# Performance work log

Measured on AMD Instinct MI355X. Metric: run time of the kernel, lower is better.

## Reference

```python
import jax, jax.numpy as jnp
import numpy as np
import math

NUM_LAYERS = 2
NUM_HEADS = 8
D_MODEL = 256
D_FF = 4 * D_MODEL
FACTOR = 5
B, L, F_IN = 8, 2048, 32


def layer_norm(x, g, b, eps=1e-5):
    m = x.mean(-1, keepdims=True)
    v = ((x - m) ** 2).mean(-1, keepdims=True)
    return (x - m) * jax.lax.rsqrt(v + eps) * g + b


def prob_attention(q, k, v, idx):
    # q,k,v: [B,H,L,Dh]; idx: [L,S] sampled key indices per query (ProbSparse)
    Bq, H, Lq, Dh = q.shape
    u = min(FACTOR * math.ceil(math.log(Lq)), Lq)  # number of 'active' queries
    k_s = k[:, :, idx, :]                              # [B,H,L,S,Dh] gathered keys
    qk_s = jnp.einsum('bhld,bhlsd->bhls', q, k_s)      # sampled scores
    M = qk_s.max(-1) - qk_s.sum(-1) / Lq               # sparsity measure [B,H,L]
    _, top = jax.lax.top_k(M, u)                       # [B,H,u] active query idx
    q_red = jnp.take_along_axis(q, top[..., None], axis=2)   # [B,H,u,Dh]
    scores = jnp.einsum('bhud,bhld->bhul', q_red, k) * (1.0 / math.sqrt(Dh))
    attn = jax.nn.softmax(scores, axis=-1)             # [B,H,u,L]
    upd = jnp.einsum('bhul,bhld->bhud', attn, v)       # [B,H,u,Dh]
    # initial context = mean of V (mask_flag=False), then scatter active rows
    ctx = jnp.broadcast_to(v.mean(2, keepdims=True), (Bq, H, Lq, Dh))
    bi = jnp.arange(Bq)[:, None, None]
    hi = jnp.arange(H)[None, :, None]
    return ctx.at[bi, hi, top].set(upd)


def setup_inputs() -> dict:
    key = jax.random.key(0)
    ks = jax.random.split(key, 16)
    S = min(FACTOR * math.ceil(math.log(L)), L)  # 40
    std = 0.02

    def w(k, shape):
        return jax.random.normal(k, shape, jnp.float32) * std

    inp = {}
    inp['x'] = jax.random.normal(ks[0], (B, L, F_IN), jnp.float32)
    inp['idx_sample'] = jax.random.randint(ks[1], (NUM_LAYERS, L, S), 0, L)
    inp['w_in'] = w(ks[2], (F_IN, D_MODEL)); inp['b_in'] = jnp.zeros((D_MODEL,), jnp.float32)
    inp['wq'] = w(ks[3], (NUM_LAYERS, D_MODEL, D_MODEL)); inp['bq'] = jnp.zeros((NUM_LAYERS, D_MODEL), jnp.float32)
    inp['wk'] = w(ks[4], (NUM_LAYERS, D_MODEL, D_MODEL)); inp['bk'] = jnp.zeros((NUM_LAYERS, D_MODEL), jnp.float32)
    inp['wv'] = w(ks[5], (NUM_LAYERS, D_MODEL, D_MODEL)); inp['bv'] = jnp.zeros((NUM_LAYERS, D_MODEL), jnp.float32)
    inp['wo'] = w(ks[6], (NUM_LAYERS, D_MODEL, D_MODEL)); inp['bo'] = jnp.zeros((NUM_LAYERS, D_MODEL), jnp.float32)
    inp['w_ff1'] = w(ks[7], (NUM_LAYERS, D_MODEL, D_FF)); inp['b_ff1'] = jnp.zeros((NUM_LAYERS, D_FF), jnp.float32)
    inp['w_ff2'] = w(ks[8], (NUM_LAYERS, D_FF, D_MODEL)); inp['b_ff2'] = jnp.zeros((NUM_LAYERS, D_MODEL), jnp.float32)
    inp['ln1_g'] = jnp.ones((NUM_LAYERS, D_MODEL), jnp.float32); inp['ln1_b'] = jnp.zeros((NUM_LAYERS, D_MODEL), jnp.float32)
    inp['ln2_g'] = jnp.ones((NUM_LAYERS, D_MODEL), jnp.float32); inp['ln2_b'] = jnp.zeros((NUM_LAYERS, D_MODEL), jnp.float32)
    inp['w_fc1'] = w(ks[9], (D_MODEL, 64)); inp['b_fc1'] = jnp.zeros((64,), jnp.float32)
    inp['w_fc2'] = w(ks[10], (64, 1)); inp['b_fc2'] = jnp.zeros((1,), jnp.float32)
    return inp


def reference(x, idx_sample, w_in, b_in, wq, bq, wk, bk, wv, bv, wo, bo,
              w_ff1, b_ff1, w_ff2, b_ff2, ln1_g, ln1_b, ln2_g, ln2_b,
              w_fc1, b_fc1, w_fc2, b_fc2):
    Bx, Lx, _ = x.shape
    h = x @ w_in + b_in  # [B,L,D_MODEL]
    for i in range(NUM_LAYERS):
        q = (h @ wq[i] + bq[i]).reshape(Bx, Lx, NUM_HEADS, -1).transpose(0, 2, 1, 3)
        k = (h @ wk[i] + bk[i]).reshape(Bx, Lx, NUM_HEADS, -1).transpose(0, 2, 1, 3)
        v = (h @ wv[i] + bv[i]).reshape(Bx, Lx, NUM_HEADS, -1).transpose(0, 2, 1, 3)
        ctx = prob_attention(q, k, v, idx_sample[i])            # [B,H,L,Dh]
        ctx = ctx.transpose(0, 2, 1, 3).reshape(Bx, Lx, D_MODEL)
        new_x = ctx @ wo[i] + bo[i]
        h = layer_norm(h + new_x, ln1_g[i], ln1_b[i])
        y = jax.nn.relu(h @ w_ff1[i] + b_ff1[i]) @ w_ff2[i] + b_ff2[i]
        h = layer_norm(h + y, ln2_g[i], ln2_b[i])
    last = h[:, -1, :]                      # take final time step
    out = jax.nn.relu(last @ w_fc1 + b_fc1) @ w_fc2 + b_fc2
    return out[:, None, :]                  # unsqueeze(1) -> [B,1,output_size]
```

## Files before the change

### kernel.cpp

```cpp
#include <hip/hip_runtime.h>
#include <math.h>

#define BB 8
#define LL 2048
#define DM 256
#define NH 8
#define DH 32
#define DFF 1024
#define SS 40
#define UU 40
#define BL (BB*LL)
#define NSL 8

typedef unsigned short ushort_t;
typedef __attribute__((ext_vector_type(8))) short short8;
typedef __attribute__((ext_vector_type(4))) float f32x4;

__device__ inline ushort_t f2b(float f)
{
    unsigned int u = __float_as_uint(f);
    u += 0x7fff + ((u >> 16) & 1);
    return (ushort_t)(u >> 16);
}

__device__ inline void gload16(const void* g, const void* l)
{
    __builtin_amdgcn_global_load_lds(
        (const __attribute__((address_space(1))) unsigned int*)g,
        (__attribute__((address_space(3))) unsigned int*)l, 16, 0, 0);
}

template<int RELU, int OUT_MODE>
__global__ __launch_bounds__(256)
void gemm_mfma(const ushort_t* __restrict__ A, const ushort_t* __restrict__ Bt,
               const float* __restrict__ bias, void* __restrict__ Cout,
               void* __restrict__ aux, int M, int N, int K)
{
    __shared__ ushort_t Asl[128 * 32];
    __shared__ ushort_t Bsl[128 * 32];

    const int t    = threadIdx.x;
    const int lane = t & 63;
    const int wv   = t >> 6;
    const int row0 = blockIdx.x * 128;
    const int col0 = blockIdx.y * 128;
    const int wr   = (wv >> 1) * 64;
    const int wc   = (wv & 1) * 64;
    const int quad = lane >> 4;
    const int l16  = lane & 15;

    f32x4 acc[4][4];
    #pragma unroll
    for (int i = 0; i < 4; ++i)
        #pragma unroll
        for (int j = 0; j < 4; ++j)
            acc[i][j] = 0.f;

    for (int k0 = 0; k0 < K; k0 += 32) {
        __syncthreads();
        #pragma unroll
        for (int r = 0; r < 2; ++r) {
            int g = r * 256 + t;
            const ushort_t* ga = A  + (size_t)(row0 + (g >> 2)) * K + k0 + (g & 3) * 8;
            const ushort_t* gb = Bt + (size_t)(col0 + (g >> 2)) * K + k0 + (g & 3) * 8;
            int lbase = (r * 256 + wv * 64) * 16;
            gload16(ga, (const char*)Asl + lbase);
            gload16(gb, (const char*)Bsl + lbase);
        }
        __syncthreads();

        short8 af[4], bfr[4];
        #pragma unroll
        for (int mi = 0; mi < 4; ++mi)
            af[mi] = *(const short8*)&Asl[(wr + mi * 16 + l16) * 32 + quad * 8];
        #pragma unroll
        for (int ni = 0; ni < 4; ++ni)
            bfr[ni] = *(const short8*)&Bsl[(wc + ni * 16 + l16) * 32 + quad * 8];
        #pragma unroll
        for (int mi = 0; mi < 4; ++mi)
            #pragma unroll
            for (int ni = 0; ni < 4; ++ni)
                acc[mi][ni] = __builtin_amdgcn_mfma_f32_16x16x32_bf16(
                    af[mi], bfr[ni], acc[mi][ni], 0, 0, 0);
    }

    #pragma unroll
    for (int mi = 0; mi < 4; ++mi) {
        #pragma unroll
        for (int ni = 0; ni < 4; ++ni) {
            int col = col0 + wc + ni * 16 + l16;
            float bb = bias[col];
            #pragma unroll
            for (int r = 0; r < 4; ++r) {
                int row = row0 + wr + mi * 16 + quad * 4 + r;
                float v = acc[mi][ni][r] + bb;
                if (RELU) v = v > 0.f ? v : 0.f;
                if (OUT_MODE == 0) {
                    ((float*)Cout)[(size_t)row * N + col] = v;
                } else if (OUT_MODE == 1) {
                    int tensor = col >> 8;
                    int c2 = col & 255;
                    int b  = row >> 11, l = row & (LL - 1);
                    int hh = c2 >> 5,  dh = c2 & 31;
                    int bh = b * NH + hh;
                    size_t bi = (((size_t)bh * LL + l) << 5) + dh;
                    ((float*)Cout)[(size_t)tensor * (BB*NH*LL*DH) + bi] = v;
                    if (tensor == 1)
                        ((ushort_t*)aux)[(((size_t)l << 6) + bh) * 32 + dh] = f2b(v);
                } else if (OUT_MODE == 2) {
                    ((ushort_t*)Cout)[(size_t)row * N + col] = f2b(v);
                } else {
                    ((float*)Cout)[(size_t)row * N + col] = v;
                    ((ushort_t*)aux)[(size_t)row * N + col] = f2b(v);
                }
            }
        }
    }
}

__global__ __launch_bounds__(256)
void gemmln_k(const ushort_t* __restrict__ A, const ushort_t* __restrict__ Bt,
              const float* __restrict__ bias, float* __restrict__ h,
              ushort_t* __restrict__ hb, const float* __restrict__ g,
              const float* __restrict__ beta, int K)
{
    __shared__ ushort_t Asl[32 * 32];
    __shared__ ushort_t Bsl[256 * 32];
    __shared__ float rs[4][32], rs2[4][32];

    const int t    = threadIdx.x;
    const int lane = t & 63;
    const int wv   = t >> 6;
    const int row0 = blockIdx.x * 32;
    const int wc   = wv * 64;
    const int quad = lane >> 4;
    const int l16  = lane & 15;

    f32x4 acc[2][4];
    #pragma unroll
    for (int i = 0; i < 2; ++i)
        #pragma unroll
        for (int j = 0; j < 4; ++j)
            acc[i][j] = 0.f;

    for (int k0 = 0; k0 < K; k0 += 32) {
        __syncthreads();
        if (wv < 2) {
            const ushort_t* ga = A + (size_t)(row0 + (t >> 2)) * K + k0 + (t & 3) * 8;
            gload16(ga, (const char*)Asl + wv * 1024);
        }
        #pragma unroll
        for (int r = 0; r < 4; ++r) {
            int gg = r * 256 + t;
            const ushort_t* gb = Bt + (size_t)(gg >> 2) * K + k0 + (gg & 3) * 8;
            gload16(gb, (const char*)Bsl + (r * 256 + wv * 64) * 16);
        }
        __syncthreads();

        short8 af[2], bfr[4];
        #pragma unroll
        for (int mi = 0; mi < 2; ++mi)
            af[mi] = *(const short8*)&Asl[(mi * 16 + l16) * 32 + quad * 8];
        #pragma unroll
        for (int ni = 0; ni < 4; ++ni)
            bfr[ni] = *(const short8*)&Bsl[(wc + ni * 16 + l16) * 32 + quad * 8];
        #pragma unroll
        for (int mi = 0; mi < 2; ++mi)
            #pragma unroll
            for (int ni = 0; ni < 4; ++ni)
                acc[mi][ni] = __builtin_amdgcn_mfma_f32_16x16x32_bf16(
                    af[mi], bfr[ni], acc[mi][ni], 0, 0, 0);
    }

    float gcol[4], bcol[4];
    #pragma unroll
    for (int ni = 0; ni < 4; ++ni) {
        int col = wc + ni * 16 + l16;
        gcol[ni] = g[col];
        bcol[ni] = beta[col];
    }
    float ps[2][4], ps2[2][4];
    #pragma unroll
    for (int mi = 0; mi < 2; ++mi) {
        #pragma unroll
        for (int r = 0; r < 4; ++r) {
            int row = row0 + mi * 16 + quad * 4 + r;
            float s = 0.f, s2 = 0.f;
            #pragma unroll
            for (int ni = 0; ni < 4; ++ni) {
                int col = wc + ni * 16 + l16;
                float v = acc[mi][ni][r] + bias[col] + h[(size_t)row * DM + col];
                acc[mi][ni][r] = v;
                s += v;
                s2 += v * v;
            }
            ps[mi][r] = s;
            ps2[mi][r] = s2;
        }
    }
    #pragma unroll
    for (int off = 1; off < 16; off <<= 1) {
        #pragma unroll
        for (int mi = 0; mi < 2; ++mi)
            #pragma unroll
            for (int r = 0; r < 4; ++r) {
                ps[mi][r]  += __shfl_xor(ps[mi][r],  off, 16);
                ps2[mi][r] += __shfl_xor(ps2[mi][r], off, 16);
            }
    }
    if (l16 == 0) {
        #pragma unroll
        for (int mi = 0; mi < 2; ++mi)
            #pragma unroll
            for (int r = 0; r < 4; ++r) {
                int lrow = mi * 16 + quad * 4 + r;
                rs[wv][lrow]  = ps[mi][r];
                rs2[wv][lrow] = ps2[mi][r];
            }
    }
    __syncthreads();

    #pragma unroll
    for (int mi = 0; mi < 2; ++mi) {
        #pragma unroll
        for (int r = 0; r < 4; ++r) {
            int lrow = mi * 16 + quad * 4 + r;
            int row  = row0 + lrow;
            float tot  = rs[0][lrow] + rs[1][lrow] + rs[2][lrow] + rs[3][lrow];
            float tot2 = rs2[0][lrow] + rs2[1][lrow] + rs2[2][lrow] + rs2[3][lrow];
            float mean = tot * (1.f / (float)DM);
            float var  = tot2 * (1.f / (float)DM) - mean * mean;
            float inv  = 1.0f / sqrtf(var + 1e-5f);
            #pragma unroll
            for (int ni = 0; ni < 4; ++ni) {
                int col = wc + ni * 16 + l16;
                float val = (acc[mi][ni][r] - mean) * inv * gcol[ni] + bcol[ni];
                h[(size_t)row * DM + col]  = val;
                hb[(size_t)row * DM + col] = f2b(val);
            }
        }
    }
}

__device__ inline void tcvt_dev(float (*tile)[33], const float* __restrict__ src,
                                ushort_t* __restrict__ dst, int K, int N,
                                int matStride, int bi)
{
    int tilesN = N >> 5;
    int tpm = (K >> 5) * tilesN;
    int m   = bi / tpm;
    int tid = bi % tpm;
    int k0 = (tid / tilesN) << 5, n0 = (tid % tilesN) << 5;
    const float* s = src + (size_t)m * K * N;
    ushort_t*    d = dst + (size_t)m * matStride;
    int r = threadIdx.x >> 5, c = threadIdx.x & 31;
    #pragma unroll
    for (int i = 0; i < 4; ++i)
        tile[r + 8 * i][c] = s[(size_t)(k0 + r + 8 * i) * N + n0 + c];
    __syncthreads();
    #pragma unroll
    for (int i = 0; i < 4; ++i)
        d[(size_t)(n0 + r + 8 * i) * K + k0 + c] = f2b(tile[c][r + 8 * i]);
}

__global__ __launch_bounds__(256)
void preproc_k(const float* __restrict__ wq, const float* __restrict__ wk,
               const float* __restrict__ wv, const float* __restrict__ wo,
               const float* __restrict__ wf1, const float* __restrict__ wf2,
               const float* __restrict__ w_in,
               const float* __restrict__ bq, const float* __restrict__ bk,
               const float* __restrict__ bv, const float* __restrict__ x,
               ushort_t* __restrict__ wqkvT, ushort_t* __restrict__ woT,
               ushort_t* __restrict__ wf1T, ushort_t* __restrict__ wf2T,
               ushort_t* __restrict__ w_inT, float* __restrict__ bqkv,
               ushort_t* __restrict__ xb16)
{
    __shared__ float tile[32][33];
    int b = blockIdx.x;
    if (b < 512) {
        int which = b >> 7, lb = b & 127;
        const float* src = which == 0 ? wq : which == 1 ? wk : which == 2 ? wv : wo;
        ushort_t* dst = which == 0 ? wqkvT : which == 1 ? wqkvT + 65536
                       : which == 2 ? wqkvT + 131072 : woT;
        int stride = which == 3 ? 65536 : 768 * 256;
        tcvt_dev(tile, src, dst, DM, DM, stride, lb);
    } else if (b < 1024) {
        tcvt_dev(tile, wf1, wf1T, DM, DFF, 1024 * 256, b - 512);
    } else if (b < 1536) {
        tcvt_dev(tile, wf2, wf2T, DFF, DM, 256 * 1024, b - 1024);
    } else if (b < 1544) {
        tcvt_dev(tile, w_in, w_inT, 32, DM, 256 * 32, b - 1536);
    } else if (b < 1550) {
        int t = (b - 1544) * 256 + threadIdx.x;
        int i = t / 768, j = t % 768;
        const float* s = j < 256 ? bq : (j < 512 ? bk : bv);
        bqkv[t] = s[i * 256 + (j & 255)];
    } else {
        int tid = (b - 1550) * 256 + threadIdx.x;
        float4 v = ((const float4*)x)[tid];
        unsigned int lo = f2b(v.x) | ((unsigned int)f2b(v.y) << 16);
        unsigned int hi = f2b(v.z) | ((unsigned int)f2b(v.w) << 16);
        ((uint2*)xb16)[tid] = make_uint2(lo, hi);
    }
}

__global__ __launch_bounds__(256)
void metric2_k(const float* __restrict__ qb, const ushort_t* __restrict__ kT,
               const int* __restrict__ idx, float* __restrict__ Mout)
{
    __shared__ float mst[64][5];
    int t = threadIdx.x;
    int w = t >> 6, lane = t & 63;
    int l = blockIdx.x * 4 + w;

    const float4* qr = (const float4*)(qb + ((size_t)(lane * LL + l) << 5));
    float4 q[8];
    #pragma unroll
    for (int i = 0; i < 8; ++i) q[i] = qr[i];

    int r40 = idx[l * SS + (lane < SS ? lane : SS - 1)];

    float mx = -3e38f, sm = 0.f;
    for (int s = 0; s < SS; ++s) {
        int r = __shfl(r40, s, 64);
        const uint4* kr = (const uint4*)(kT + (((size_t)r << 6) + lane) * 32);
        float d = 0.f;
        #pragma unroll
        for (int ww = 0; ww < 4; ++ww) {
            uint4 kv = kr[ww];
            float4 qa = q[2 * ww], qb2 = q[2 * ww + 1];
            d = fmaf(__uint_as_float(kv.x << 16),         qa.x, d);
            d = fmaf(__uint_as_float(kv.x & 0xffff0000u), qa.y, d);
            d = fmaf(__uint_as_float(kv.y << 16),         qa.z, d);
            d = fmaf(__uint_as_float(kv.y & 0xffff0000u), qa.w, d);
            d = fmaf(__uint_as_float(kv.z << 16),         qb2.x, d);
            d = fmaf(__uint_as_float(kv.z & 0xffff0000u), qb2.y, d);
            d = fmaf(__uint_as_float(kv.w << 16),         qb2.z, d);
            d = fmaf(__uint_as_float(kv.w & 0xffff0000u), qb2.w, d);
        }
        mx = fmaxf(mx, d);
        sm += d;
    }
    mst[lane][w] = mx - sm * (1.0f / (float)LL);
    __syncthreads();

    int bh = t >> 2, ls = t & 3;
    Mout[(size_t)bh * LL + blockIdx.x * 4 + ls] = mst[bh][ls];
}

__global__ __launch_bounds__(256)
void topk1_k(const float* __restrict__ Mout,
             float* __restrict__ cand_v, int* __restrict__ cand_i)
{
    int lane = threadIdx.x & 63;
    int slg  = blockIdx.x * 4 + (threadIdx.x >> 6);
    int bh   = slg >> 3;
    int l0   = (slg & 7) << 8;

    float v[4];
    #pragma unroll
    for (int i = 0; i < 4; ++i)
        v[i] = Mout[(size_t)bh * LL + l0 + i * 64 + lane];

    for (int r = 0; r < UU; ++r) {
        float bv = -3e38f; int bi = 1 << 30;
        #pragma unroll
        for (int i = 0; i < 4; ++i) {
            int idx = l0 + i * 64 + lane;
            if (v[i] > bv || (v[i] == bv && idx < bi)) { bv = v[i]; bi = idx; }
        }
        #pragma unroll
        for (int off = 32; off > 0; off >>= 1) {
            float ov = __shfl_down(bv, off, 64);
            int   oi = __shfl_down(bi, off, 64);
            if (ov > bv || (ov == bv && oi < bi)) { bv = ov; bi = oi; }
        }
        bv = __shfl(bv, 0, 64);
        bi = __shfl(bi, 0, 64);
        if (lane == 0) {
            cand_v[slg * UU + r] = bv;
            cand_i[slg * UU + r] = bi;
        }
        int rel = bi - l0;
        if ((rel & 63) == lane) v[rel >> 6] = -3e38f;
    }
}

__global__ __launch_bounds__(256)
void topk2_k(const float* __restrict__ cand_v, const int* __restrict__ cand_i,
             int* __restrict__ top)
{
    __shared__ float cv[320];
    __shared__ int   ci[320];
    int bh = blockIdx.x, t = threadIdx.x;
    for (int i = t; i < 320; i += 256) {
        cv[i] = cand_v[bh * 320 + i];
        ci[i] = cand_i[bh * 320 + i];
    }
    __syncthreads();
    for (int c = t; c < 320; c += 256) {
        float mv = cv[c]; int mi = ci[c];
        int rank = 0;
        for (int j = 0; j < 320; ++j)
            rank += (cv[j] > mv) || (cv[j] == mv && ci[j] < mi);
        if (rank < UU) top[bh * UU + rank] = mi;
    }
}

__global__ __launch_bounds__(256)
void vmeanp_k(const float* __restrict__ vb, float* __restrict__ vmeP)
{
    __shared__ float red[8][32];
    int blk = blockIdx.x;
    int bh = blk >> 3, sl = blk & 7;
    int t = threadIdx.x;
    int d = t & 31, part = t >> 5;
    const float* base = vb + ((size_t)(bh * LL + sl * 256 + part * 32) << 5);
    float s = 0.f;
    #pragma unroll 8
    for (int i = 0; i < 32; ++i) s += base[(i << 5) + d];
    red[part][d] = s;
    __syncthreads();
    if (t < 32) {
        float tot = 0.f;
        #pragma unroll
        for (int p = 0; p < 8; ++p) tot += red[p][t];
        vmeP[blk * 32 + t] = tot;
    }
}

__global__ __launch_bounds__(256)
void vfin_k(const float* __restrict__ vmeP, float* __restrict__ vme)
{
    int tid = blockIdx.x * 256 + threadIdx.x;
    int bh = tid >> 5, d = tid & 31;
    float s = 0.f;
    #pragma unroll
    for (int sl = 0; sl < 8; ++sl) s += vmeP[(bh * 8 + sl) * 32 + d];
    vme[tid] = s * (1.f / (float)LL);
}

__global__ __launch_bounds__(256)
void attnupd_k(const float* __restrict__ qb, const float* __restrict__ kb,
               const float* __restrict__ vb, const int* __restrict__ top,
               float* __restrict__ mP, float* __restrict__ sP,
               float* __restrict__ OP)
{
    __shared__ float qs[UU * 32];
    __shared__ float sc[UU * 256];
    __shared__ float msh[UU];

    int blk = blockIdx.x;
    int sl  = blk & (NSL - 1);
    int bh  = blk >> 3;
    int t   = threadIdx.x;
    int l0  = sl << 8;

    for (int i = t; i < UU * 32; i += 256) {
        int j = i >> 5, dd = i & 31;
        qs[i] = qb[((size_t)(bh * LL + top[bh * UU + j]) << 5) + dd];
    }

    const float4* kr = (const float4*)(kb + ((size_t)(bh * LL + l0 + t) << 5));
    float4 k4[8];
    #pragma unroll
    for (int i = 0; i < 8; ++i) k4[i] = kr[i];
    __syncthreads();

    const float scale = 0.17677669529663687f;
    #pragma unroll 4
    for (int j = 0; j < UU; ++j) {
        float ds = 0.f;
        #pragma unroll
        for (int i = 0; i < 8; ++i) {
            float4 qv = *(const float4*)&qs[j * 32 + 4 * i];
            ds = fmaf(qv.x, k4[i].x, ds);
            ds = fmaf(qv.y, k4[i].y, ds);
            ds = fmaf(qv.z, k4[i].z, ds);
            ds = fmaf(qv.w, k4[i].w, ds);
        }
        sc[j * 256 + t] = ds * scale;
    }
    __syncthreads();

    int j8 = t >> 5, d = t & 31;
    #pragma unroll
    for (int g = 0; g < 5; ++g) {
        int j = g * 8 + j8;
        float4 a = *(const float4*)&sc[j * 256 + 4 * d];
        float4 b = *(const float4*)&sc[j * 256 + 128 + 4 * d];
        float m = fmaxf(fmaxf(fmaxf(a.x, a.y), fmaxf(a.z, a.w)),
                        fmaxf(fmaxf(b.x, b.y), fmaxf(b.z, b.w)));
        #pragma unroll
        for (int off = 16; off > 0; off >>= 1)
            m = fmaxf(m, __shfl_down(m, off, 64));
        if (d == 0) msh[j] = m;
    }
    __syncthreads();

    #pragma unroll 8
    for (int i = t; i < UU * 256; i += 256) {
        int j = i >> 8;
        sc[i] = __expf(sc[i] - msh[j]);
    }
    __syncthreads();

    int pq = bh * NSL + sl;

    #pragma unroll
    for (int g = 0; g < 5; ++g) {
        int j = g * 8 + j8;
        float4 a = *(const float4*)&sc[j * 256 + 4 * d];
        float4 b = *(const float4*)&sc[j * 256 + 128 + 4 * d];
        float s = a.x + a.y + a.z + a.w + b.x + b.y + b.z + b.w;
        #pragma unroll
        for (int off = 16; off > 0; off >>= 1)
            s += __shfl_down(s, off, 64);
        if (d == 0) { sP[pq * UU + j] = s; mP[pq * UU + j] = msh[j]; }
    }

    const float* vbase = vb + ((size_t)(bh * LL + l0) << 5) + d;
    float acc[5] = {0.f, 0.f, 0.f, 0.f, 0.f};
    #pragma unroll 4
    for (int i = 0; i < 64; ++i) {
        float v0 = vbase[(4 * i + 0) << 5];
        float v1 = vbase[(4 * i + 1) << 5];
        float v2 = vbase[(4 * i + 2) << 5];
        float v3 = vbase[(4 * i + 3) << 5];
        #pragma unroll
        for (int g = 0; g < 5; ++g) {
            float4 e4 = *(const float4*)&sc[(g * 8 + j8) * 256 + 4 * i];
            acc[g] = fmaf(e4.x, v0, acc[g]);
            acc[g] = fmaf(e4.y, v1, acc[g]);
            acc[g] = fmaf(e4.z, v2, acc[g]);
            acc[g] = fmaf(e4.w, v3, acc[g]);
        }
    }
    #pragma unroll
    for (int g = 0; g < 5; ++g)
        OP[((size_t)pq * UU + g * 8 + j8) * 32 + d] = acc[g];
}

__global__ __launch_bounds__(256)
void combine_k(const float* __restrict__ mP, const float* __restrict__ sP,
               const float* __restrict__ OP, const int* __restrict__ top,
               ushort_t* __restrict__ ctxb)
{
    int tid = blockIdx.x * 256 + threadIdx.x;
    int d  = tid & 31;
    int j  = (tid >> 5) % UU;
    int bh = tid / (UU * 32);
    float M = -3e38f;
    #pragma unroll
    for (int q = 0; q < NSL; ++q) M = fmaxf(M, mP[(bh * NSL + q) * UU + j]);
    float S = 0.f, O = 0.f;
    #pragma unroll
    for (int q = 0; q < NSL; ++q) {
        float w = __expf(mP[(bh * NSL + q) * UU + j] - M);
        S = fmaf(sP[(bh * NSL + q) * UU + j], w, S);
        O = fmaf(OP[((size_t)(bh * NSL + q) * UU + j) * 32 + d], w, O);
    }
    float u = O / S;
    int qi = top[bh * UU + j];
    int b = bh >> 3, hh = bh & 7;
    ctxb[(((size_t)(b * LL + qi)) << 8) + (hh << 5) + d] = f2b(u);
}

__global__ __launch_bounds__(256)
void fill2_k(ushort_t* __restrict__ ctxb, const float* __restrict__ vmean)
{
    int tid = blockIdx.x * 256 + threadIdx.x;
    int pr = tid & 127;
    int b  = tid >> 18;
    float v0 = vmean[(b << 8) + pr * 2];
    float v1 = vmean[(b << 8) + pr * 2 + 1];
    ((unsigned int*)ctxb)[tid] = (unsigned int)f2b(v0) | ((unsigned int)f2b(v1) << 16);
}

__global__ __launch_bounds__(512)
void head_k(const float* __restrict__ h, const float* __restrict__ w1,
            const float* __restrict__ b1, const float* __restrict__ w2,
            const float* __restrict__ b2, float* __restrict__ out)
{
    int t = threadIdx.x;
    int b = t >> 6, j = t & 63;
    const float* hr = h + ((size_t)(b * LL + (LL - 1))) * DM;
    float s = 0.f;
    for (int kk = 0; kk < DM; ++kk) s = fmaf(hr[kk], w1[kk * 64 + j], s);
    s += b1[j];
    s = s > 0.f ? s : 0.f;
    float contrib = s * w2[j];
    #pragma unroll
    for (int off = 32; off > 0; off >>= 1) contrib += __shfl_down(contrib, off);
    if (j == 0) out[b] = contrib + b2[0];
}

extern "C" void kernel_launch(void* const* d_in, const int* in_sizes, int n_in,
                              void* d_out, int out_size, void* d_ws, size_t ws_size,
                              hipStream_t stream)
{
    const float* x    = (const float*)d_in[0];
    const int*   idx  = (const int*)  d_in[1];
    const float* w_in = (const float*)d_in[2];
    const float* b_in = (const float*)d_in[3];
    const float* wq   = (const float*)d_in[4];
    const float* bq   = (const float*)d_in[5];
    const float* wk   = (const float*)d_in[6];
    const float* bk   = (const float*)d_in[7];
    const float* wv   = (const float*)d_in[8];
    const float* bv   = (const float*)d_in[9];
    const float* wo   = (const float*)d_in[10];
    const float* bo   = (const float*)d_in[11];
    const float* wf1  = (const float*)d_in[12];
    const float* bf1  = (const float*)d_in[13];
    const float* wf2  = (const float*)d_in[14];
    const float* bf2  = (const float*)d_in[15];
    const float* g1   = (const float*)d_in[16];
    const float* be1  = (const float*)d_in[17];
    const float* g2   = (const float*)d_in[18];
    const float* be2  = (const float*)d_in[19];
    const float* wfc1 = (const float*)d_in[20];
    const float* bfc1 = (const float*)d_in[21];
    const float* wfc2 = (const float*)d_in[22];
    const float* bfc2 = (const float*)d_in[23];
    float* out = (float*)d_out;

    float* ws = (float*)d_ws;
    float*    h     = ws;
    float*    qkv   = ws + 4194304;
    float*    qb    = qkv;
    float*    kb    = qkv + 4194304;
    float*    vb    = qkv + 8388608;
    float*    attnS = ws + 16777216;
    ushort_t* kT16  = (ushort_t*)attnS;
    float*    Mbuf  = attnS + 2097152;
    float*    candv = attnS + 2228224;
    int*      candi = (int*)(attnS + 2248704);
    float*    vmeP  = attnS + 2269184;
    float*    OP    = attnS + 2285568;
    float*    mP    = attnS + 2940928;
    float*    sP    = attnS + 2961408;
    float*    scr   = ws + 20971520;
    ushort_t* xb16  = (ushort_t*)scr;
    float*    vme   = scr + 262144;
    int*      top   = (int*)(scr + 264192);
    ushort_t* hb    = (ushort_t*)(scr + 266752);
    ushort_t* wqkvT = (ushort_t*)(scr + 2363904);
    ushort_t* woT   = (ushort_t*)(scr + 2560512);
    ushort_t* wf1T  = (ushort_t*)(scr + 2626048);
    ushort_t* wf2T  = (ushort_t*)(scr + 2888192);
    ushort_t* w_inT = (ushort_t*)(scr + 3150336);
    float*    bqkv  = scr + 3154432;
    ushort_t* ctxb  = (ushort_t*)qkv;
    ushort_t* ffbb  = (ushort_t*)(qkv + 2097152);

    dim3 blk(256);

    preproc_k<<<dim3(2062), blk, 0, stream>>>(
        wq, wk, wv, wo, wf1, wf2, w_in, bq, bk, bv, x,
        wqkvT, woT, wf1T, wf2T, w_inT, bqkv, xb16);

    gemm_mfma<0,3><<<dim3(BL/128, 2), blk, 0, stream>>>(
        xb16, w_inT, b_in, (void*)h, (void*)hb, BL, DM, 32);

    for (int i = 0; i < 2; ++i) {
        gemm_mfma<0,1><<<dim3(BL/128, 6), blk, 0, stream>>>(
            hb, wqkvT + (size_t)i*768*256, bqkv + i*768, (void*)qkv, (void*)kT16,
            BL, 768, DM);

        metric2_k<<<dim3(512), blk, 0, stream>>>(qb, kT16, idx + (size_t)i*LL*SS, Mbuf);
        topk1_k<<<dim3(128), blk, 0, stream>>>(Mbuf, candv, candi);
        topk2_k<<<dim3(BB*NH), blk, 0, stream>>>(candv, candi, top);
        vmeanp_k<<<dim3(512), blk, 0, stream>>>(vb, vmeP);
        vfin_k<<<dim3(8), blk, 0, stream>>>(vmeP, vme);
        attnupd_k<<<dim3(BB*NH*NSL), blk, 0, stream>>>(qb, kb, vb, top, mP, sP, OP);

        fill2_k<<<dim3(BL*DM/512), blk, 0, stream>>>(ctxb, vme);
        combine_k<<<dim3(BB*NH*UU*DH/256), blk, 0, stream>>>(mP, sP, OP, top, ctxb);

        gemmln_k<<<dim3(BL/32), blk, 0, stream>>>(
            ctxb, woT + (size_t)i*256*256, bo + i*DM, h, hb,
            g1 + i*DM, be1 + i*DM, DM);

        gemm_mfma<1,2><<<dim3(BL/128, 8), blk, 0, stream>>>(
            hb, wf1T + (size_t)i*1024*256, bf1 + i*DFF, (void*)ffbb, nullptr, BL, DFF, DM);

        gemmln_k<<<dim3(BL/32), blk, 0, stream>>>(
            ffbb, wf2T + (size_t)i*256*1024, bf2 + i*DM, h, hb,
            g2 + i*DM, be2 + i*DM, DFF);
    }

    head_k<<<dim3(1), dim3(512), 0, stream>>>(h, wfc1, bfc1, wfc2, bfc2, out);
}
```

Baseline: 519.0 us.

## Fuse top-k, V-mean, fill/combine and output head into fewer kernels

```diff
diff --git a/kernel.cpp b/kernel.cpp
--- a/kernel.cpp
+++ b/kernel.cpp
@@ -13,6 +13,7 @@
 #define NSL 8
 
 typedef unsigned short ushort_t;
+typedef unsigned char uchar_t;
 typedef __attribute__((ext_vector_type(8))) short short8;
 typedef __attribute__((ext_vector_type(4))) float f32x4;
 
@@ -118,15 +119,20 @@
     }
 }
 
+template<int HEAD>
 __global__ __launch_bounds__(256)
 void gemmln_k(const ushort_t* __restrict__ A, const ushort_t* __restrict__ Bt,
               const float* __restrict__ bias, float* __restrict__ h,
               ushort_t* __restrict__ hb, const float* __restrict__ g,
-              const float* __restrict__ beta, int K)
+              const float* __restrict__ beta, int K,
+              const float* __restrict__ w1, const float* __restrict__ b1,
+              const float* __restrict__ w2, const float* __restrict__ b2,
+              float* __restrict__ out)
 {
     __shared__ ushort_t Asl[32 * 32];
     __shared__ ushort_t Bsl[256 * 32];
     __shared__ float rs[4][32], rs2[4][32];
+    __shared__ float hrowS[256];
 
     const int t    = threadIdx.x;
     const int lane = t & 63;
@@ -237,7 +243,25 @@
                 float val = (acc[mi][ni][r] - mean) * inv * gcol[ni] + bcol[ni];
                 h[(size_t)row * DM + col]  = val;
                 hb[(size_t)row * DM + col] = f2b(val);
+                if (HEAD && lrow == 31) hrowS[col] = val;
             }
+        }
+    }
+
+    if (HEAD) {
+        __syncthreads();
+        if ((blockIdx.x & 63) == 63 && t < 64) {
+            int b = blockIdx.x >> 6;
+            float s = 0.f;
+            for (int kk = 0; kk < DM; ++kk)
+                s = fmaf(hrowS[kk], w1[kk * 64 + t], s);
+            s += b1[t];
+            s = s > 0.f ? s : 0.f;
+            float contrib = s * w2[t];
+            #pragma unroll
+            for (int off = 32; off > 0; off >>= 1)
+                contrib += __shfl_down(contrib, off, 64);
+            if (t == 0) out[b] = contrib + b2[0];
         }
     }
 }
@@ -306,12 +330,19 @@
 
 __global__ __launch_bounds__(256)
 void metric2_k(const float* __restrict__ qb, const ushort_t* __restrict__ kT,
-               const int* __restrict__ idx, float* __restrict__ Mout)
+               const int* __restrict__ idx, float* __restrict__ Mout,
+               unsigned int* __restrict__ jidx32)
 {
     __shared__ float mst[64][5];
     int t = threadIdx.x;
     int w = t >> 6, lane = t & 63;
     int l = blockIdx.x * 4 + w;
+
+    if (t < 64) {
+        int zb = t >> 3, sel = t & 7;
+        int zl = blockIdx.x * 4 + (sel >> 1), half = sel & 1;
+        jidx32[(size_t)(zb * LL + zl) * 2 + half] = 0;
+    }
 
     const float4* qr = (const float4*)(qb + ((size_t)(lane * LL + l) << 5));
     float4 q[8];
@@ -349,95 +380,73 @@
 }
 
 __global__ __launch_bounds__(256)
-void topk1_k(const float* __restrict__ Mout,
-             float* __restrict__ cand_v, int* __restrict__ cand_i)
-{
-    int lane = threadIdx.x & 63;
-    int slg  = blockIdx.x * 4 + (threadIdx.x >> 6);
-    int bh   = slg >> 3;
-    int l0   = (slg & 7) << 8;
-
-    float v[4];
-    #pragma unroll
-    for (int i = 0; i < 4; ++i)
-        v[i] = Mout[(size_t)bh * LL + l0 + i * 64 + lane];
-
-    for (int r = 0; r < UU; ++r) {
-        float bv = -3e38f; int bi = 1 << 30;
-        #pragma unroll
-        for (int i = 0; i < 4; ++i) {
-            int idx = l0 + i * 64 + lane;
-            if (v[i] > bv || (v[i] == bv && idx < bi)) { bv = v[i]; bi = idx; }
-        }
-        #pragma unroll
-        for (int off = 32; off > 0; off >>= 1) {
-            float ov = __shfl_down(bv, off, 64);
-            int   oi = __shfl_down(bi, off, 64);
-            if (ov > bv || (ov == bv && oi < bi)) { bv = ov; bi = oi; }
-        }
-        bv = __shfl(bv, 0, 64);
-        bi = __shfl(bi, 0, 64);
-        if (lane == 0) {
-            cand_v[slg * UU + r] = bv;
-            cand_i[slg * UU + r] = bi;
-        }
-        int rel = bi - l0;
-        if ((rel & 63) == lane) v[rel >> 6] = -3e38f;
-    }
-}
-
-__global__ __launch_bounds__(256)
-void topk2_k(const float* __restrict__ cand_v, const int* __restrict__ cand_i,
-             int* __restrict__ top)
-{
-    __shared__ float cv[320];
-    __shared__ int   ci[320];
-    int bh = blockIdx.x, t = threadIdx.x;
-    for (int i = t; i < 320; i += 256) {
-        cv[i] = cand_v[bh * 320 + i];
-        ci[i] = cand_i[bh * 320 + i];
-    }
-    __syncthreads();
+void selectvm_k(const float* __restrict__ Mout, const float* __restrict__ vb,
+                int* __restrict__ top, uchar_t* __restrict__ jidx,
+                float* __restrict__ vme)
+{
+    __shared__ float cvS[320];
+    __shared__ int   ciS[320];
+    __shared__ float red[8][32];
+
+    int bh = blockIdx.x;
+    int t  = threadIdx.x;
+    int lane = t & 63, w = t >> 6;
+
+    for (int ss = 0; ss < 2; ++ss) {
+        int sl = w * 2 + ss;
+        int l0 = sl << 8;
+        float v[4];
+        #pragma unroll
+        for (int i = 0; i < 4; ++i)
+            v[i] = Mout[(size_t)bh * LL + l0 + i * 64 + lane];
+
+        for (int r = 0; r < UU; ++r) {
+            float bv = -3e38f; int bi = 1 << 30;
+            #pragma unroll
+            for (int i = 0; i < 4; ++i) {
+                int idx = l0 + i * 64 + lane;
+                if (v[i] > bv || (v[i] == bv && idx < bi)) { bv = v[i]; bi = idx; }
+            }
+            #pragma unroll
+            for (int off = 32; off > 0; off >>= 1) {
+                float ov = __shfl_down(bv, off, 64);
+                int   oi = __shfl_down(bi, off, 64);
+                if (ov > bv || (ov == bv && oi < bi)) { bv = ov; bi = oi; }
+            }
+            bv = __shfl(bv, 0, 64);
+            bi = __shfl(bi, 0, 64);
+            if (lane == 0) { cvS[sl * UU + r] = bv; ciS[sl * UU + r] = bi; }
+            int rel = bi - l0;
+            if ((rel & 63) == lane) v[rel >> 6] = -3e38f;
+        }
+    }
+    __syncthreads();
+
     for (int c = t; c < 320; c += 256) {
-        float mv = cv[c]; int mi = ci[c];
+        float mv = cvS[c]; int mi = ciS[c];
         int rank = 0;
         for (int j = 0; j < 320; ++j)
-            rank += (cv[j] > mv) || (cv[j] == mv && ci[j] < mi);
-        if (rank < UU) top[bh * UU + rank] = mi;
-    }
-}
-
-__global__ __launch_bounds__(256)
-void vmeanp_k(const float* __restrict__ vb, float* __restrict__ vmeP)
-{
-    __shared__ float red[8][32];
-    int blk = blockIdx.x;
-    int bh = blk >> 3, sl = blk & 7;
-    int t = threadIdx.x;
+            rank += (cvS[j] > mv) || (cvS[j] == mv && ciS[j] < mi);
+        if (rank < UU) {
+            top[bh * UU + rank] = mi;
+            int b = bh >> 3, hh = bh & 7;
+            jidx[(size_t)(b * LL + mi) * 8 + hh] = (uchar_t)(rank + 1);
+        }
+    }
+
     int d = t & 31, part = t >> 5;
-    const float* base = vb + ((size_t)(bh * LL + sl * 256 + part * 32) << 5);
+    const float* base = vb + ((size_t)bh * LL << 5);
     float s = 0.f;
-    #pragma unroll 8
-    for (int i = 0; i < 32; ++i) s += base[(i << 5) + d];
+    int l0 = part * 256;
+    for (int i = 0; i < 256; ++i) s += base[((size_t)(l0 + i) << 5) + d];
     red[part][d] = s;
     __syncthreads();
     if (t < 32) {
         float tot = 0.f;
         #pragma unroll
         for (int p = 0; p < 8; ++p) tot += red[p][t];
-        vmeP[blk * 32 + t] = tot;
-    }
-}
-
-__global__ __launch_bounds__(256)
-void vfin_k(const float* __restrict__ vmeP, float* __restrict__ vme)
-{
-    int tid = blockIdx.x * 256 + threadIdx.x;
-    int bh = tid >> 5, d = tid & 31;
-    float s = 0.f;
-    #pragma unroll
-    for (int sl = 0; sl < 8; ++sl) s += vmeP[(bh * 8 + sl) * 32 + d];
-    vme[tid] = s * (1.f / (float)LL);
+        vme[bh * 32 + t] = tot * (1.f / (float)LL);
+    }
 }
 
 __global__ __launch_bounds__(256)
@@ -542,57 +551,40 @@
 }
 
 __global__ __launch_bounds__(256)
-void combine_k(const float* __restrict__ mP, const float* __restrict__ sP,
-               const float* __restrict__ OP, const int* __restrict__ top,
-               ushort_t* __restrict__ ctxb)
+void fillcomb_k(const float* __restrict__ vme, const uchar_t* __restrict__ jidx,
+                const float* __restrict__ mP, const float* __restrict__ sP,
+                const float* __restrict__ OP, ushort_t* __restrict__ ctxb)
 {
     int tid = blockIdx.x * 256 + threadIdx.x;
-    int d  = tid & 31;
-    int j  = (tid >> 5) % UU;
-    int bh = tid / (UU * 32);
-    float M = -3e38f;
-    #pragma unroll
-    for (int q = 0; q < NSL; ++q) M = fmaxf(M, mP[(bh * NSL + q) * UU + j]);
-    float S = 0.f, O = 0.f;
-    #pragma unroll
-    for (int q = 0; q < NSL; ++q) {
-        float w = __expf(mP[(bh * NSL + q) * UU + j] - M);
-        S = fmaf(sP[(bh * NSL + q) * UU + j], w, S);
-        O = fmaf(OP[((size_t)(bh * NSL + q) * UU + j) * 32 + d], w, O);
-    }
-    float u = O / S;
-    int qi = top[bh * UU + j];
-    int b = bh >> 3, hh = bh & 7;
-    ctxb[(((size_t)(b * LL + qi)) << 8) + (hh << 5) + d] = f2b(u);
-}
-
-__global__ __launch_bounds__(256)
-void fill2_k(ushort_t* __restrict__ ctxb, const float* __restrict__ vmean)
-{
-    int tid = blockIdx.x * 256 + threadIdx.x;
-    int pr = tid & 127;
-    int b  = tid >> 18;
-    float v0 = vmean[(b << 8) + pr * 2];
-    float v1 = vmean[(b << 8) + pr * 2 + 1];
+    int pr   = tid & 127;
+    int rowi = tid >> 7;
+    int b    = rowi >> 11;
+    int hh   = pr >> 4;
+    int j    = (int)jidx[(size_t)rowi * 8 + hh];
+
+    float v0, v1;
+    if (j == 0) {
+        v0 = vme[(b << 8) + pr * 2];
+        v1 = vme[(b << 8) + pr * 2 + 1];
+    } else {
+        int jj = j - 1;
+        int bh = b * 8 + hh;
+        int d0 = (pr * 2) & 31;
+        float M = -3e38f;
+        #pragma unroll
+        for (int q = 0; q < NSL; ++q) M = fmaxf(M, mP[(bh * NSL + q) * UU + jj]);
+        float S = 0.f, O0 = 0.f, O1 = 0.f;
+        #pragma unroll
+        for (int q = 0; q < NSL; ++q) {
+            float wgt = __expf(mP[(bh * NSL + q) * UU + jj] - M);
+            S  = fmaf(sP[(bh * NSL + q) * UU + jj], wgt, S);
+            O0 = fmaf(OP[((size_t)(bh * NSL + q) * UU + jj) * 32 + d0], wgt, O0);
+            O1 = fmaf(OP[((size_t)(bh * NSL + q) * UU + jj) * 32 + d0 + 1], wgt, O1);
+        }
+        v0 = O0 / S;
+        v1 = O1 / S;
+    }
     ((unsigned int*)ctxb)[tid] = (unsigned int)f2b(v0) | ((unsigned int)f2b(v1) << 16);
-}
-
-__global__ __launch_bounds__(512)
-void head_k(const float* __restrict__ h, const float* __restrict__ w1,
-            const float* __restrict__ b1, const float* __restrict__ w2,
-            const float* __restrict__ b2, float* __restrict__ out)
-{
-    int t = threadIdx.x;
-    int b = t >> 6, j = t & 63;
-    const float* hr = h + ((size_t)(b * LL + (LL - 1))) * DM;
-    float s = 0.f;
-    for (int kk = 0; kk < DM; ++kk) s = fmaf(hr[kk], w1[kk * 64 + j], s);
-    s += b1[j];
-    s = s > 0.f ? s : 0.f;
-    float contrib = s * w2[j];
-    #pragma unroll
-    for (int off = 32; off > 0; off >>= 1) contrib += __shfl_down(contrib, off);
-    if (j == 0) out[b] = contrib + b2[0];
 }
 
 extern "C" void kernel_launch(void* const* d_in, const int* in_sizes, int n_in,
@@ -634,12 +626,10 @@
     float*    attnS = ws + 16777216;
     ushort_t* kT16  = (ushort_t*)attnS;
     float*    Mbuf  = attnS + 2097152;
-    float*    candv = attnS + 2228224;
-    int*      candi = (int*)(attnS + 2248704);
-    float*    vmeP  = attnS + 2269184;
     float*    OP    = attnS + 2285568;
     float*    mP    = attnS + 2940928;
     float*    sP    = attnS + 2961408;
+    uchar_t*  jidx  = (uchar_t*)(attnS + 2981888);
     float*    scr   = ws + 20971520;
     ushort_t* xb16  = (ushort_t*)scr;
     float*    vme   = scr + 262144;
@@ -668,27 +658,30 @@
             hb, wqkvT + (size_t)i*768*256, bqkv + i*768, (void*)qkv, (void*)kT16,
             BL, 768, DM);
 
-        metric2_k<<<dim3(512), blk, 0, stream>>>(qb, kT16, idx + (size_t)i*LL*SS, Mbuf);
-        topk1_k<<<dim3(128), blk, 0, stream>>>(Mbuf, candv, candi);
-        topk2_k<<<dim3(BB*NH), blk, 0, stream>>>(candv, candi, top);
-        vmeanp_k<<<dim3(512), blk, 0, stream>>>(vb, vmeP);
-        vfin_k<<<dim3(8), blk, 0, stream>>>(vmeP, vme);
+        metric2_k<<<dim3(512), blk, 0, stream>>>(
+            qb, kT16, idx + (size_t)i*LL*SS, Mbuf, (unsigned int*)jidx);
+        selectvm_k<<<dim3(BB*NH), blk, 0, stream>>>(Mbuf, vb, top, jidx, vme);
         attnupd_k<<<dim3(BB*NH*NSL), blk, 0, stream>>>(qb, kb, vb, top, mP, sP, OP);
-
-        fill2_k<<<dim3(BL*DM/512), blk, 0, stream>>>(ctxb, vme);
-        combine_k<<<dim3(BB*NH*UU*DH/256), blk, 0, stream>>>(mP, sP, OP, top, ctxb);
-
-        gemmln_k<<<dim3(BL/32), blk, 0, stream>>>(
+        fillcomb_k<<<dim3(BL*DM/512), blk, 0, stream>>>(vme, jidx, mP, sP, OP, ctxb);
+
+        gemmln_k<0><<<dim3(BL/32), blk, 0, stream>>>(
             ctxb, woT + (size_t)i*256*256, bo + i*DM, h, hb,
-            g1 + i*DM, be1 + i*DM, DM);
+            g1 + i*DM, be1 + i*DM, DM,
+            nullptr, nullptr, nullptr, nullptr, nullptr);
 
         gemm_mfma<1,2><<<dim3(BL/128, 8), blk, 0, stream>>>(
             hb, wf1T + (size_t)i*1024*256, bf1 + i*DFF, (void*)ffbb, nullptr, BL, DFF, DM);
 
-        gemmln_k<<<dim3(BL/32), blk, 0, stream>>>(
-            ffbb, wf2T + (size_t)i*256*1024, bf2 + i*DM, h, hb,
-            g2 + i*DM, be2 + i*DM, DFF);
-    }
-
-    head_k<<<dim3(1), dim3(512), 0, stream>>>(h, wfc1, bfc1, wfc2, bfc2, out);
-}
+        if (i == 1) {
+            gemmln_k<1><<<dim3(BL/32), blk, 0, stream>>>(
+                ffbb, wf2T + (size_t)i*256*1024, bf2 + i*DM, h, hb,
+                g2 + i*DM, be2 + i*DM, DFF,
+                wfc1, bfc1, wfc2, bfc2, out);
+        } else {
+            gemmln_k<0><<<dim3(BL/32), blk, 0, stream>>>(
+                ffbb, wf2T + (size_t)i*256*1024, bf2 + i*DM, h, hb,
+                g2 + i*DM, be2 + i*DM, DFF,
+                nullptr, nullptr, nullptr, nullptr, nullptr);
+        }
+    }
+}
```

After: 563.7 us. 8.6% more time.
